# Kernel tuning notes

Hardware: AMD Instinct MI355X
Metric: run time of the kernel (lower is better)

Reference implementation:

```python
import jax, jax.numpy as jnp
import numpy as np

HEADS = 24
HEAD_DIM = 96
SPARSE_N = 4
ROPE_BASE = 10000.0


def _rope_cos_sin(pos, D):
    # pos: [L] int positions; D: per-axis rotary dim (even)
    inv_freq = 1.0 / (ROPE_BASE ** (jnp.arange(0, D, 2, dtype=jnp.float32) / D))
    f = pos.astype(jnp.float32)[:, None] * inv_freq[None, :]   # [L, D/2] (interp scale = 1)
    f = jnp.concatenate([f, f], axis=-1)                        # [L, D]
    return jnp.cos(f), jnp.sin(f)


def _rotate_half(x):
    x1, x2 = jnp.split(x, 2, axis=-1)
    return jnp.concatenate([-x2, x1], axis=-1)


def _apply_rope3d(tok, frame, height, width):
    # tok: [b, h, s, d]; RoPE3D splits head_dim into 3 equal chunks for (t, y, x)
    D = tok.shape[-1] // 3
    t = jnp.repeat(jnp.arange(frame), height * width)
    y = jnp.tile(jnp.repeat(jnp.arange(height), width), frame)
    x = jnp.tile(jnp.arange(width), frame * height)
    outs = []
    for i, pos in enumerate((t, y, x)):
        cos, sin = _rope_cos_sin(pos, D)                        # [s, D]
        part = tok[..., i * D:(i + 1) * D]
        outs.append(part * cos[None, None] + _rotate_half(part) * sin[None, None])
    return jnp.concatenate(outs, axis=-1)


def _sparse_1d(x, n):
    # 'b h (g k) d -> (k b) h g d' with pad so s % n*n == 0
    b, h, s, d = x.shape
    pad = (-s) % (n * n)
    if pad:
        x = jnp.pad(x, ((0, 0), (0, 0), (0, pad), (0, 0)))
    g = (s + pad) // n
    x = x.reshape(b, h, g, n, d)
    return jnp.transpose(x, (3, 0, 1, 2, 4)).reshape(n * b, h, g, d), pad


def _reverse_sparse_1d(x, n, s):
    # '(k b) h g d -> b h (g k) d' then crop to s tokens
    kb, h, g, d = x.shape
    b = kb // n
    x = x.reshape(n, b, h, g, d)
    x = jnp.transpose(x, (1, 2, 3, 0, 4)).reshape(b, h, g * n, d)
    return x[:, :, :s, :]


def setup_inputs() -> dict:
    key = jax.random.key(0)
    ks = jax.random.split(key, 5)
    dim = HEADS * HEAD_DIM
    b, f, hh, ww = 1, 8, 16, 32
    s = f * hh * ww
    inp = {
        "hidden_states": jax.random.normal(ks[0], (b, s, dim), dtype=jnp.float32),
        "wq": jax.random.normal(ks[1], (dim, dim), dtype=jnp.float32) * 0.02,
        "bq": jnp.zeros((dim,), jnp.float32),
        "wk": jax.random.normal(ks[2], (dim, dim), dtype=jnp.float32) * 0.02,
        "bk": jnp.zeros((dim,), jnp.float32),
        "wv": jax.random.normal(ks[3], (dim, dim), dtype=jnp.float32) * 0.02,
        "bv": jnp.zeros((dim,), jnp.float32),
        "wo": jax.random.normal(ks[4], (dim, dim), dtype=jnp.float32) * 0.02,
        "bo": jnp.zeros((dim,), jnp.float32),
        "frame": f, "height": hh, "width": ww,
    }
    return inp


def reference(hidden_states, wq, bq, wk, bk, wv, bv, wo, bo, frame, height, width):
    b, s, dim = hidden_states.shape
    assert s == frame * height * width

    def proj(w, bias):
        y = hidden_states @ w + bias                            # [b, s, dim]
        return jnp.transpose(y.reshape(b, s, HEADS, HEAD_DIM), (0, 2, 1, 3))  # [b, h, s, d]

    q = proj(wq, bq)
    k = proj(wk, bk)
    v = proj(wv, bv)

    # 3D rotary embedding on q, k (self-attention path)
    q = _apply_rope3d(q, frame, height, width)
    k = _apply_rope3d(k, frame, height, width)

    # sparse-1d grouping (sparse_group=False): strided token groups of size s/sparse_n
    q, _ = _sparse_1d(q, SPARSE_N)
    k, _ = _sparse_1d(k, SPARSE_N)
    v, _ = _sparse_1d(v, SPARSE_N)

    scale = 1.0 / jnp.sqrt(jnp.asarray(HEAD_DIM, jnp.float32))
    scores = jnp.einsum('bhqd,bhkd->bhqk', q, k) * scale        # [(n b), h, g, g]
    probs = jax.nn.softmax(scores, axis=-1)
    out = jnp.einsum('bhqk,bhkd->bhqd', probs, v)

    out = _reverse_sparse_1d(out, SPARSE_N, s)                   # [b, h, s, d]
    out = jnp.transpose(out, (0, 2, 1, 3)).reshape(b, s, dim)
    return out @ wo + bo
```

## Files before the change

kernel.cpp:

```cpp
#include <hip/hip_runtime.h>
#include <stdint.h>

#define S_TOK 4096
#define DIM   2304
#define NH    24
#define DH    96
#define GQ    1024
#define KDIM  2304

typedef unsigned short ushort_t;
typedef __attribute__((ext_vector_type(8))) short bf16x8;
typedef __attribute__((ext_vector_type(4))) float f32x4;

__device__ __forceinline__ ushort_t f2bf(float x) {
    union { float f; uint32_t u; } c; c.f = x;
    uint32_t u = c.u + 0x7FFFu + ((c.u >> 16) & 1u);
    return (ushort_t)(u >> 16);
}

#define GLDS(gp, lp) __builtin_amdgcn_global_load_lds( \
    (const __attribute__((address_space(1))) void*)(gp), \
    (__attribute__((address_space(3))) void*)(lp), 16, 0, 0)

__global__ __launch_bounds__(256) void cast_bf16_kernel(const float* __restrict__ in,
                                                        ushort_t* __restrict__ out, int n4) {
    int i = blockIdx.x * 256 + threadIdx.x;
    if (i >= n4) return;
    float4 v = ((const float4*)in)[i];
    ushort4 o;
    o.x = f2bf(v.x); o.y = f2bf(v.y); o.z = f2bf(v.z); o.w = f2bf(v.w);
    ((ushort4*)out)[i] = o;
}

__global__ __launch_bounds__(256) void wtrans_kernel(const float* __restrict__ W0,
                                                     const float* __restrict__ W1,
                                                     const float* __restrict__ W2,
                                                     const float* __restrict__ W3,
                                                     ushort_t* __restrict__ WT0, int dim) {
    __shared__ float tile[32][33];
    const int z = blockIdx.z;
    const float* W = (z == 0) ? W0 : (z == 1) ? W1 : (z == 2) ? W2 : W3;
    ushort_t* WT = WT0 + (size_t)z * dim * dim;
    const int bx = blockIdx.x * 32;
    const int by = blockIdx.y * 32;
    const int tx = threadIdx.x & 31, ty = threadIdx.x >> 5;
#pragma unroll
    for (int i = 0; i < 4; ++i)
        tile[ty + i*8][tx] = W[(size_t)(by + ty + i*8) * dim + bx + tx];
    __syncthreads();
#pragma unroll
    for (int i = 0; i < 4; ++i)
        WT[(size_t)(bx + ty + i*8) * dim + by + tx] = f2bf(tile[tx][ty + i*8]);
}

template<bool FINAL>
__global__ __launch_bounds__(512, 2) void gemm256(const ushort_t* __restrict__ A,
                                                  const ushort_t* __restrict__ Bt,
                                                  const float* __restrict__ bq,
                                                  const float* __restrict__ bk,
                                                  const float* __restrict__ bv,
                                                  ushort_t* __restrict__ Qb,
                                                  ushort_t* __restrict__ Kb,
                                                  ushort_t* __restrict__ Vtb,
                                                  float* __restrict__ Cf) {
    constexpr int K  = KDIM;
    constexpr int NT = K / 32;
    __shared__ ushort_t a_s[4 * 8192];
    __shared__ ushort_t b_s[4 * 8192];
    const int t = threadIdx.x, l = t & 63, w = t >> 6;
    const int wr = w >> 2, wc = w & 3, g = l >> 4, ln = l & 15;
    const int nwg = gridDim.x * gridDim.y;
    const int lin = blockIdx.y * gridDim.x + blockIdx.x;
    const int cpx = nwg >> 3;
    const int swz = (lin & 7) * cpx + (lin >> 3);
    const int bx = swz % gridDim.x, by = swz / gridDim.x;
    const int m0 = by * 256, n0 = bx * 256;

    const int swz_rd = (g ^ ((ln >> 1) & 3)) * 8;
    const int kc_src = (((t & 3) ^ ((t >> 3) & 3)) * 8);
    const int srow   = t >> 2;

    auto stageA = [&](int kt) {
        const int slot = kt & 3;
#pragma unroll
        for (int q = 0; q < 2; ++q)
            GLDS(A + (size_t)(m0 + q*128 + srow) * K + kt*32 + kc_src,
                 &a_s[slot*8192 + (q*512 + t) * 8]);
    };
    auto stageB = [&](int kt) {
        const int slot = kt & 3;
#pragma unroll
        for (int q = 0; q < 2; ++q)
            GLDS(Bt + (size_t)(n0 + q*128 + srow) * K + kt*32 + kc_src,
                 &b_s[slot*8192 + (q*512 + t) * 8]);
    };

    f32x4 acc[8][4] = {};

    stageA(0); stageB(0); stageA(1); stageB(1); stageA(2); stageB(2);
    asm volatile("s_waitcnt vmcnt(8)" ::: "memory");
    __builtin_amdgcn_s_barrier();

    for (int kt = 0; kt < NT; ++kt) {
        const int slot = kt & 3;
        bf16x8 bv4[4];
        {
            bf16x8 av[4];
#pragma unroll
            for (int j = 0; j < 4; ++j)
                bv4[j] = *(const bf16x8*)&b_s[slot*8192 + (wc*64 + j*16 + ln)*32 + swz_rd];
#pragma unroll
            for (int i = 0; i < 4; ++i)
                av[i] = *(const bf16x8*)&a_s[slot*8192 + (wr*128 + i*16 + ln)*32 + swz_rd];
            if (kt < NT - 3) stageA(kt + 3);
            __builtin_amdgcn_s_barrier();
            asm volatile("s_waitcnt lgkmcnt(0)" ::: "memory");
            __builtin_amdgcn_sched_barrier(0);
            __builtin_amdgcn_s_setprio(1);
#pragma unroll
            for (int i = 0; i < 4; ++i)
#pragma unroll
                for (int j = 0; j < 4; ++j)
                    acc[i][j] = __builtin_amdgcn_mfma_f32_16x16x32_bf16(av[i], bv4[j], acc[i][j], 0, 0, 0);
            __builtin_amdgcn_s_setprio(0);
        }
        {
            bf16x8 av[4];
#pragma unroll
            for (int i = 0; i < 4; ++i)
                av[i] = *(const bf16x8*)&a_s[slot*8192 + (wr*128 + 64 + i*16 + ln)*32 + swz_rd];
            if (kt < NT - 3) stageB(kt + 3);
            if (kt <= NT - 4)      asm volatile("s_waitcnt vmcnt(8)" ::: "memory");
            else if (kt == NT - 3) asm volatile("s_waitcnt vmcnt(4)" ::: "memory");
            else                   asm volatile("s_waitcnt vmcnt(0)" ::: "memory");
            __builtin_amdgcn_s_barrier();
            asm volatile("s_waitcnt lgkmcnt(0)" ::: "memory");
            __builtin_amdgcn_sched_barrier(0);
            __builtin_amdgcn_s_setprio(1);
#pragma unroll
            for (int i = 0; i < 4; ++i)
#pragma unroll
                for (int j = 0; j < 4; ++j)
                    acc[4 + i][j] = __builtin_amdgcn_mfma_f32_16x16x32_bf16(av[i], bv4[j], acc[4 + i][j], 0, 0, 0);
            __builtin_amdgcn_s_setprio(0);
        }
    }

    if constexpr (FINAL) {
        const float* bias = bq;
#pragma unroll
        for (int i = 0; i < 8; ++i) {
            int mb = m0 + wr*128 + i*16 + g*4;
#pragma unroll
            for (int j = 0; j < 4; ++j) {
                int n = n0 + wc*64 + j*16 + ln;
                float bb = bias[n];
#pragma unroll
                for (int r = 0; r < 4; ++r)
                    Cf[(size_t)(mb + r) * DIM + n] = acc[i][j][r] + bb;
            }
        }
    } else {
        const int mode = bx / 9;
        const int nb = (bx - mode * 9) * 256;
        const float* bias = (mode == 0) ? bq : (mode == 1) ? bk : bv;
        if (mode == 2) {
#pragma unroll
            for (int i = 0; i < 8; ++i) {
                int mb = m0 + wr*128 + i*16 + g*4;
                int q  = mb >> 2;
#pragma unroll
                for (int j = 0; j < 4; ++j) {
                    int nm = nb + wc*64 + j*16 + ln;
                    int hh = nm / DH, d = nm - hh * DH;
                    float bb = bias[nm];
#pragma unroll
                    for (int r = 0; r < 4; ++r)
                        Vtb[(size_t)(r * NH + hh) * (DH * GQ) + (size_t)d * GQ + q] =
                            f2bf(acc[i][j][r] + bb);
                }
            }
        } else {
            ushort_t* O = (mode == 0) ? Qb : Kb;
            const float scq = (mode == 0) ? 0.1472444635222742f : 1.0f;
#pragma unroll
            for (int i = 0; i < 8; ++i) {
                int mb = m0 + wr*128 + i*16 + g*4;
#pragma unroll
                for (int jp = 0; jp < 2; ++jp) {
                    int j  = jp * 2;
                    int n1 = nb + wc*64 + j*16 + ln;
                    int hh = n1 / DH, d1 = n1 - hh * DH;
                    int sec = d1 >> 5, f = d1 & 15;
                    float invf = __expf((float)f * -0.5756462732485114f);
                    float b1 = bias[n1], b2 = bias[n1 + 16];
#pragma unroll
                    for (int r = 0; r < 4; ++r) {
                        int m = mb + r;
                        int pos = (sec == 0) ? (m >> 9) : (sec == 1) ? ((m >> 5) & 15) : (m & 31);
                        float ang = (float)pos * invf;
                        float sn, cs;
                        __sincosf(ang, &sn, &cs);
                        float v1 = acc[i][j][r]     + b1;
                        float v2 = acc[i][j + 1][r] + b2;
                        size_t base = ((size_t)((m & 3) * NH + hh)) * (GQ * DH) + (size_t)(m >> 2) * DH;
                        O[base + d1]      = f2bf((v1 * cs - v2 * sn) * scq);
                        O[base + d1 + 16] = f2bf((v2 * cs + v1 * sn) * scq);
                    }
                }
            }
        }
    }
}

__global__ __launch_bounds__(256) void gemm128(const ushort_t* __restrict__ A,
                                               const ushort_t* __restrict__ Bt,
                                               const float* __restrict__ bias,
                                               float* __restrict__ C) {
    constexpr int K  = KDIM;
    constexpr int NT = K / 32;
    __shared__ ushort_t a_s[2 * 4096];
    __shared__ ushort_t b_s[2 * 4096];
    const int t = threadIdx.x;
    const int l = t & 63, w = t >> 6;
    const int wr = w >> 1, wc = w & 1;
    const int g = l >> 4, ln = l & 15;
    const int lin = blockIdx.y * gridDim.x + blockIdx.x;
    const int swz = (lin & 7) * 72 + (lin >> 3);
    const int bx = swz % 18, by = swz / 18;
    const int m0 = by * 128, n0 = bx * 128;

    const int swz_rd = (g ^ ((ln >> 1) & 3)) * 8;
    const int kc_src = (((t & 3) ^ ((t >> 3) & 3)) * 8);
    const int srow   = t >> 2;

    const ushort_t* Ab = A  + (size_t)(m0 + srow) * K + kc_src;
    const ushort_t* Bb = Bt + (size_t)(n0 + srow) * K + kc_src;
    const size_t rstep = (size_t)64 * K;

    auto stage = [&](int kt) {
        const int slot = kt & 1;
        GLDS(Ab + kt*32,         &a_s[slot*4096 + t*8]);
        GLDS(Ab + rstep + kt*32, &a_s[slot*4096 + 2048 + t*8]);
        GLDS(Bb + kt*32,         &b_s[slot*4096 + t*8]);
        GLDS(Bb + rstep + kt*32, &b_s[slot*4096 + 2048 + t*8]);
    };

    f32x4 acc[4][4] = {};

    stage(0); stage(1);
    asm volatile("s_waitcnt vmcnt(4)" ::: "memory");
    __builtin_amdgcn_s_barrier();

    for (int kt = 0; kt < NT; ++kt) {
        const int slot = kt & 1;
        bf16x8 av[4], bv[4];
#pragma unroll
        for (int i = 0; i < 4; ++i)
            av[i] = *(const bf16x8*)&a_s[slot*4096 + (wr*64 + i*16 + ln) * 32 + swz_rd];
#pragma unroll
        for (int j = 0; j < 4; ++j)
            bv[j] = *(const bf16x8*)&b_s[slot*4096 + (wc*64 + j*16 + ln) * 32 + swz_rd];
        asm volatile("s_waitcnt lgkmcnt(0)" ::: "memory");
        __builtin_amdgcn_sched_barrier(0);
        __builtin_amdgcn_s_barrier();
        if (kt < NT - 2) {
            stage(kt + 2);
            asm volatile("s_waitcnt vmcnt(4)" ::: "memory");
        } else {
            asm volatile("s_waitcnt vmcnt(0)" ::: "memory");
        }
        __builtin_amdgcn_sched_barrier(0);
        __builtin_amdgcn_s_setprio(1);
#pragma unroll
        for (int i = 0; i < 4; ++i)
#pragma unroll
            for (int j = 0; j < 4; ++j)
                acc[i][j] = __builtin_amdgcn_mfma_f32_16x16x32_bf16(av[i], bv[j], acc[i][j], 0, 0, 0);
        __builtin_amdgcn_s_setprio(0);
        __builtin_amdgcn_sched_barrier(0);
        __builtin_amdgcn_s_barrier();
    }

#pragma unroll
    for (int i = 0; i < 4; ++i) {
        int mb = m0 + wr*64 + i*16 + g*4;
#pragma unroll
        for (int j = 0; j < 4; ++j) {
            int n = n0 + wc*64 + j*16 + ln;
            float bb = bias[n];
#pragma unroll
            for (int r = 0; r < 4; ++r)
                C[(size_t)(mb + r) * DIM + n] = acc[i][j][r] + bb;
        }
    }
}

__global__ __launch_bounds__(256, 3) void attn_kernel(const ushort_t* __restrict__ Qb,
                                                      const ushort_t* __restrict__ Kb,
                                                      const ushort_t* __restrict__ Vt,
                                                      ushort_t* __restrict__ ATT) {
    __shared__ ushort_t k_s[2][12 * 64 * 8];
    __shared__ ushort_t v_s[8 * 96 * 8];
    __shared__ ushort_t p_s[4 * 2 * 16 * 64];

    const int t = threadIdx.x, l = t & 63, w = t >> 6, g = l >> 4, ln = l & 15;
    const int lin  = blockIdx.x;
    const int swz  = (lin & 7) * 96 + (lin >> 3);
    const int inst = swz >> 3;
    const int qb0  = (swz & 7) * 128;
    const int n_idx = inst / NH, h = inst - n_idx * NH;
    const int swzp = (ln & 7) << 3;

    const ushort_t* Qi = Qb + (size_t)inst * (GQ * DH);
    const ushort_t* Ki = Kb + (size_t)inst * (GQ * DH);
    const ushort_t* Vi = Vt + (size_t)inst * (DH * GQ);

    auto stageK = [&](int kt, int b) {
#pragma unroll
        for (int it = 0; it < 3; ++it) {
            int P = t + it * 256;
            int c = P >> 6, key = P & 63;
            GLDS(Ki + (size_t)(kt * 64 + key) * DH + c * 8, &k_s[b][P * 8]);
        }
    };
    auto stageV = [&](int kt) {
#pragma unroll
        for (int it = 0; it < 3; ++it) {
            int P = t + it * 256;
            int c = P / 96, d = P - c * 96;
            GLDS(Vi + (size_t)d * GQ + kt * 64 + c * 8, &v_s[P * 8]);
        }
    };

    bf16x8 qf[2][3];
#pragma unroll
    for (int qt = 0; qt < 2; ++qt)
#pragma unroll
        for (int ks = 0; ks < 3; ++ks)
            qf[qt][ks] = *(const bf16x8*)(Qi + (size_t)(qb0 + w*32 + qt*16 + ln) * DH + ks*32 + g*8);

    float m_run[2], l_run[2];
#pragma unroll
    for (int qt = 0; qt < 2; ++qt) { m_run[qt] = -3.0e38f; l_run[qt] = 0.f; }
    f32x4 acc_o[2][6] = {};

    stageK(0, 0);
    stageV(0);
    __syncthreads();

    int cur = 0;
    for (int kt = 0; kt < 16; ++kt) {
        stageK((kt + 1) & 15, cur ^ 1);
        float al2[2];
        bool grew[2];

        f32x4 sc[2][4] = {};
        __builtin_amdgcn_s_setprio(1);
#pragma unroll
        for (int ct = 0; ct < 4; ++ct) {
            bf16x8 kf0 = *(const bf16x8*)&k_s[cur][((0*4 + g)*64 + ct*16 + ln) * 8];
            bf16x8 kf1 = *(const bf16x8*)&k_s[cur][((1*4 + g)*64 + ct*16 + ln) * 8];
            bf16x8 kf2 = *(const bf16x8*)&k_s[cur][((2*4 + g)*64 + ct*16 + ln) * 8];
#pragma unroll
            for (int qi = 0; qi < 2; ++qi) {
                sc[qi][ct] = __builtin_amdgcn_mfma_f32_16x16x32_bf16(kf0, qf[qi][0], sc[qi][ct], 0, 0, 0);
                sc[qi][ct] = __builtin_amdgcn_mfma_f32_16x16x32_bf16(kf1, qf[qi][1], sc[qi][ct], 0, 0, 0);
                sc[qi][ct] = __builtin_amdgcn_mfma_f32_16x16x32_bf16(kf2, qf[qi][2], sc[qi][ct], 0, 0, 0);
            }
        }
        __builtin_amdgcn_s_setprio(0);
#pragma unroll
        for (int qi = 0; qi < 2; ++qi) {
            const int qt = qi;
            float mx = sc[qi][0][0];
#pragma unroll
            for (int ct = 0; ct < 4; ++ct)
#pragma unroll
                for (int r = 0; r < 4; ++r)
                    mx = fmaxf(mx, sc[qi][ct][r]);
            mx = fmaxf(mx, __shfl_xor(mx, 16, 64));
            mx = fmaxf(mx, __shfl_xor(mx, 32, 64));
            bool grow = !__all(mx <= m_run[qt]);
            float al = 1.0f;
            if (grow) {
                float mn = fmaxf(m_run[qt], mx);
                al = __builtin_amdgcn_exp2f(m_run[qt] - mn);
                m_run[qt] = mn;
            }
            grew[qi] = grow;
            float rs = 0.f;
            ushort_t pb[16];
#pragma unroll
            for (int ct = 0; ct < 4; ++ct)
#pragma unroll
                for (int r = 0; r < 4; ++r) {
                    float p = __builtin_amdgcn_exp2f(sc[qi][ct][r] - m_run[qt]);
                    rs += p;
                    pb[ct*4 + r] = f2bf(p);
                }
            rs += __shfl_xor(rs, 16, 64);
            rs += __shfl_xor(rs, 32, 64);
            l_run[qt] = l_run[qt] * al + rs;
            al2[qt] = al;
            const int pbase = ((w*2 + qt)*16 + ln) * 64;
#pragma unroll
            for (int ct = 0; ct < 4; ++ct) {
                ushort4 pk;
                pk.x = pb[ct*4+0]; pk.y = pb[ct*4+1]; pk.z = pb[ct*4+2]; pk.w = pb[ct*4+3];
                *(ushort4*)&p_s[pbase + ((ct*16 + g*4) ^ swzp)] = pk;
            }
        }

        if (grew[0] || grew[1]) {
#pragma unroll
            for (int qt = 0; qt < 2; ++qt)
#pragma unroll
                for (int r = 0; r < 4; ++r) {
                    float a = __shfl(al2[qt], g*4 + r, 16);
#pragma unroll
                    for (int dt = 0; dt < 6; ++dt)
                        acc_o[qt][dt][r] *= a;
                }
        }

        asm volatile("s_waitcnt vmcnt(3)" ::: "memory");
        __builtin_amdgcn_s_barrier();
        __builtin_amdgcn_sched_barrier(0);
        asm volatile("s_waitcnt lgkmcnt(0)" ::: "memory");
        __builtin_amdgcn_sched_barrier(0);

        __builtin_amdgcn_s_setprio(1);
#pragma unroll
        for (int kb = 0; kb < 2; ++kb) {
            bf16x8 pf2[2];
#pragma unroll
            for (int qt = 0; qt < 2; ++qt)
                pf2[qt] = *(const bf16x8*)&p_s[((w*2 + qt)*16 + ln)*64 + ((kb*32 + g*8) ^ swzp)];
#pragma unroll
            for (int dt = 0; dt < 6; ++dt) {
                bf16x8 vf = *(const bf16x8*)&v_s[((kb*4 + g)*96 + dt*16 + ln) * 8];
#pragma unroll
                for (int qt = 0; qt < 2; ++qt)
                    acc_o[qt][dt] = __builtin_amdgcn_mfma_f32_16x16x32_bf16(pf2[qt], vf, acc_o[qt][dt], 0, 0, 0);
            }
        }
        __builtin_amdgcn_s_setprio(0);

        __syncthreads();
        if (kt < 15) stageV(kt + 1);
        cur ^= 1;
    }

#pragma unroll
    for (int qt = 0; qt < 2; ++qt) {
        float inv = 1.0f / l_run[qt];
#pragma unroll
        for (int r = 0; r < 4; ++r) {
            float iv = __shfl(inv, g*4 + r, 16);
            int gq = qb0 + w*32 + qt*16 + g*4 + r;
            size_t base = ((size_t)(gq * 4 + n_idx)) * DIM + h * DH;
#pragma unroll
            for (int dt = 0; dt < 6; ++dt)
                ATT[base + dt*16 + ln] = f2bf(acc_o[qt][dt][r] * iv);
        }
    }
}

extern "C" void kernel_launch(void* const* d_in, const int* in_sizes, int n_in,
                              void* d_out, int out_size, void* d_ws, size_t ws_size,
                              hipStream_t stream) {
    const float* hidden = (const float*)d_in[0];
    const float* wq = (const float*)d_in[1];
    const float* bq = (const float*)d_in[2];
    const float* wk = (const float*)d_in[3];
    const float* bk = (const float*)d_in[4];
    const float* wv = (const float*)d_in[5];
    const float* bv = (const float*)d_in[6];
    const float* wo = (const float*)d_in[7];
    const float* bo = (const float*)d_in[8];
    float* out = (float*)d_out;

    char* ws = (char*)d_ws;
    ushort_t* Xb  = (ushort_t*)ws;
    ushort_t* WTq = (ushort_t*)(ws + 18874368);
    ushort_t* WTk = WTq + (size_t)DIM * DIM;
    ushort_t* WTv = WTk + (size_t)DIM * DIM;
    ushort_t* WTo = WTv + (size_t)DIM * DIM;
    ushort_t* Qb  = WTo + (size_t)DIM * DIM;
    ushort_t* Kb  = Qb + (size_t)S_TOK * DIM;
    ushort_t* Vtb = Kb + (size_t)S_TOK * DIM;
    ushort_t* ATT = Vtb + (size_t)S_TOK * DIM;

    cast_bf16_kernel<<<dim3(9216), dim3(256), 0, stream>>>(hidden, Xb, (S_TOK * DIM) / 4);

    wtrans_kernel<<<dim3(72, 72, 4), 256, 0, stream>>>(wq, wk, wv, wo, WTq, DIM);

    gemm256<false><<<dim3(27, 16), 512, 0, stream>>>(Xb, WTq, bq, bk, bv, Qb, Kb, Vtb, nullptr);

    attn_kernel<<<dim3(768), 256, 0, stream>>>(Qb, Kb, Vtb, ATT);

    gemm128<<<dim3(18, 32), 256, 0, stream>>>(ATT, WTo, bo, out);
}
```

Before: 325.9 us.

## Replace 256x256 QKV GEMM with 128x128 tiled kernel and double buffering

The fused QKV projection GEMM moves from 256x256 tiles with 512 threads and a 4-stage LDS pipeline to 128x128 tiles with 256 threads, a 2-stage pipeline, and 4 blocks per CU. This raises the block count from 432 to 1728 so the 256 CUs are filled more evenly, with less tail imbalance. In exchange, each tile gets less operand reuse, so global and L2 traffic rises, and the shallower pipeline may hide latency less well. The RoPE, scaling and scatter epilogue is kept the same, with indices adapted to the smaller tile.

```diff
diff --git a/kernel.cpp b/kernel.cpp
--- a/kernel.cpp
+++ b/kernel.cpp
@@ -53,160 +53,124 @@
         WT[(size_t)(bx + ty + i*8) * dim + by + tx] = f2bf(tile[tx][ty + i*8]);
 }
 
-template<bool FINAL>
-__global__ __launch_bounds__(512, 2) void gemm256(const ushort_t* __restrict__ A,
-                                                  const ushort_t* __restrict__ Bt,
-                                                  const float* __restrict__ bq,
-                                                  const float* __restrict__ bk,
-                                                  const float* __restrict__ bv,
-                                                  ushort_t* __restrict__ Qb,
-                                                  ushort_t* __restrict__ Kb,
-                                                  ushort_t* __restrict__ Vtb,
-                                                  float* __restrict__ Cf) {
+__global__ __launch_bounds__(256, 4) void gemm128_qkv(const ushort_t* __restrict__ A,
+                                                      const ushort_t* __restrict__ Bt,
+                                                      const float* __restrict__ bq,
+                                                      const float* __restrict__ bk,
+                                                      const float* __restrict__ bv,
+                                                      ushort_t* __restrict__ Qb,
+                                                      ushort_t* __restrict__ Kb,
+                                                      ushort_t* __restrict__ Vtb) {
     constexpr int K  = KDIM;
     constexpr int NT = K / 32;
-    __shared__ ushort_t a_s[4 * 8192];
-    __shared__ ushort_t b_s[4 * 8192];
-    const int t = threadIdx.x, l = t & 63, w = t >> 6;
-    const int wr = w >> 2, wc = w & 3, g = l >> 4, ln = l & 15;
-    const int nwg = gridDim.x * gridDim.y;
+    __shared__ ushort_t a_s[2 * 4096];
+    __shared__ ushort_t b_s[2 * 4096];
+    const int t = threadIdx.x;
+    const int l = t & 63, w = t >> 6;
+    const int wr = w >> 1, wc = w & 1;
+    const int g = l >> 4, ln = l & 15;
     const int lin = blockIdx.y * gridDim.x + blockIdx.x;
-    const int cpx = nwg >> 3;
-    const int swz = (lin & 7) * cpx + (lin >> 3);
-    const int bx = swz % gridDim.x, by = swz / gridDim.x;
-    const int m0 = by * 256, n0 = bx * 256;
+    const int swz = (lin & 7) * 216 + (lin >> 3);
+    const int bx = swz % 54, by = swz / 54;
+    const int m0 = by * 128, n0g = bx * 128;
 
     const int swz_rd = (g ^ ((ln >> 1) & 3)) * 8;
     const int kc_src = (((t & 3) ^ ((t >> 3) & 3)) * 8);
     const int srow   = t >> 2;
 
-    auto stageA = [&](int kt) {
-        const int slot = kt & 3;
-#pragma unroll
-        for (int q = 0; q < 2; ++q)
-            GLDS(A + (size_t)(m0 + q*128 + srow) * K + kt*32 + kc_src,
-                 &a_s[slot*8192 + (q*512 + t) * 8]);
+    const ushort_t* Ab = A  + (size_t)(m0  + srow) * K + kc_src;
+    const ushort_t* Bb = Bt + (size_t)(n0g + srow) * K + kc_src;
+    const size_t rstep = (size_t)64 * K;
+
+    auto stage = [&](int kt) {
+        const int slot = kt & 1;
+        GLDS(Ab + kt*32,         &a_s[slot*4096 + t*8]);
+        GLDS(Ab + rstep + kt*32, &a_s[slot*4096 + 2048 + t*8]);
+        GLDS(Bb + kt*32,         &b_s[slot*4096 + t*8]);
+        GLDS(Bb + rstep + kt*32, &b_s[slot*4096 + 2048 + t*8]);
     };
-    auto stageB = [&](int kt) {
-        const int slot = kt & 3;
-#pragma unroll
-        for (int q = 0; q < 2; ++q)
-            GLDS(Bt + (size_t)(n0 + q*128 + srow) * K + kt*32 + kc_src,
-                 &b_s[slot*8192 + (q*512 + t) * 8]);
-    };
-
-    f32x4 acc[8][4] = {};
-
-    stageA(0); stageB(0); stageA(1); stageB(1); stageA(2); stageB(2);
-    asm volatile("s_waitcnt vmcnt(8)" ::: "memory");
+
+    f32x4 acc[4][4] = {};
+
+    stage(0); stage(1);
+    asm volatile("s_waitcnt vmcnt(4)" ::: "memory");
     __builtin_amdgcn_s_barrier();
 
     for (int kt = 0; kt < NT; ++kt) {
-        const int slot = kt & 3;
-        bf16x8 bv4[4];
-        {
-            bf16x8 av[4];
+        const int slot = kt & 1;
+        bf16x8 av[4], bv4[4];
+#pragma unroll
+        for (int i = 0; i < 4; ++i)
+            av[i] = *(const bf16x8*)&a_s[slot*4096 + (wr*64 + i*16 + ln) * 32 + swz_rd];
+#pragma unroll
+        for (int j = 0; j < 4; ++j)
+            bv4[j] = *(const bf16x8*)&b_s[slot*4096 + (wc*64 + j*16 + ln) * 32 + swz_rd];
+        asm volatile("s_waitcnt lgkmcnt(0)" ::: "memory");
+        __builtin_amdgcn_sched_barrier(0);
+        __builtin_amdgcn_s_barrier();
+        if (kt < NT - 2) {
+            stage(kt + 2);
+            asm volatile("s_waitcnt vmcnt(4)" ::: "memory");
+        } else {
+            asm volatile("s_waitcnt vmcnt(0)" ::: "memory");
+        }
+        __builtin_amdgcn_sched_barrier(0);
+        __builtin_amdgcn_s_setprio(1);
+#pragma unroll
+        for (int i = 0; i < 4; ++i)
 #pragma unroll
             for (int j = 0; j < 4; ++j)
-                bv4[j] = *(const bf16x8*)&b_s[slot*8192 + (wc*64 + j*16 + ln)*32 + swz_rd];
-#pragma unroll
-            for (int i = 0; i < 4; ++i)
-                av[i] = *(const bf16x8*)&a_s[slot*8192 + (wr*128 + i*16 + ln)*32 + swz_rd];
-            if (kt < NT - 3) stageA(kt + 3);
-            __builtin_amdgcn_s_barrier();
-            asm volatile("s_waitcnt lgkmcnt(0)" ::: "memory");
-            __builtin_amdgcn_sched_barrier(0);
-            __builtin_amdgcn_s_setprio(1);
-#pragma unroll
-            for (int i = 0; i < 4; ++i)
-#pragma unroll
-                for (int j = 0; j < 4; ++j)
-                    acc[i][j] = __builtin_amdgcn_mfma_f32_16x16x32_bf16(av[i], bv4[j], acc[i][j], 0, 0, 0);
-            __builtin_amdgcn_s_setprio(0);
-        }
-        {
-            bf16x8 av[4];
-#pragma unroll
-            for (int i = 0; i < 4; ++i)
-                av[i] = *(const bf16x8*)&a_s[slot*8192 + (wr*128 + 64 + i*16 + ln)*32 + swz_rd];
-            if (kt < NT - 3) stageB(kt + 3);
-            if (kt <= NT - 4)      asm volatile("s_waitcnt vmcnt(8)" ::: "memory");
-            else if (kt == NT - 3) asm volatile("s_waitcnt vmcnt(4)" ::: "memory");
-            else                   asm volatile("s_waitcnt vmcnt(0)" ::: "memory");
-            __builtin_amdgcn_s_barrier();
-            asm volatile("s_waitcnt lgkmcnt(0)" ::: "memory");
-            __builtin_amdgcn_sched_barrier(0);
-            __builtin_amdgcn_s_setprio(1);
-#pragma unroll
-            for (int i = 0; i < 4; ++i)
-#pragma unroll
-                for (int j = 0; j < 4; ++j)
-                    acc[4 + i][j] = __builtin_amdgcn_mfma_f32_16x16x32_bf16(av[i], bv4[j], acc[4 + i][j], 0, 0, 0);
-            __builtin_amdgcn_s_setprio(0);
-        }
-    }
-
-    if constexpr (FINAL) {
-        const float* bias = bq;
-#pragma unroll
-        for (int i = 0; i < 8; ++i) {
-            int mb = m0 + wr*128 + i*16 + g*4;
+                acc[i][j] = __builtin_amdgcn_mfma_f32_16x16x32_bf16(av[i], bv4[j], acc[i][j], 0, 0, 0);
+        __builtin_amdgcn_s_setprio(0);
+        __builtin_amdgcn_sched_barrier(0);
+        __builtin_amdgcn_s_barrier();
+    }
+
+    const int mode = bx / 18;
+    const int nb = (bx - mode * 18) * 128;
+    const float* bias = (mode == 0) ? bq : (mode == 1) ? bk : bv;
+    if (mode == 2) {
+#pragma unroll
+        for (int i = 0; i < 4; ++i) {
+            int mb = m0 + wr*64 + i*16 + g*4;
+            int q  = mb >> 2;
 #pragma unroll
             for (int j = 0; j < 4; ++j) {
-                int n = n0 + wc*64 + j*16 + ln;
-                float bb = bias[n];
+                int nm = nb + wc*64 + j*16 + ln;
+                int hh = nm / DH, d = nm - hh * DH;
+                float bb = bias[nm];
 #pragma unroll
                 for (int r = 0; r < 4; ++r)
-                    Cf[(size_t)(mb + r) * DIM + n] = acc[i][j][r] + bb;
+                    Vtb[(size_t)(r * NH + hh) * (DH * GQ) + (size_t)d * GQ + q] =
+                        f2bf(acc[i][j][r] + bb);
             }
         }
     } else {
-        const int mode = bx / 9;
-        const int nb = (bx - mode * 9) * 256;
-        const float* bias = (mode == 0) ? bq : (mode == 1) ? bk : bv;
-        if (mode == 2) {
-#pragma unroll
-            for (int i = 0; i < 8; ++i) {
-                int mb = m0 + wr*128 + i*16 + g*4;
-                int q  = mb >> 2;
-#pragma unroll
-                for (int j = 0; j < 4; ++j) {
-                    int nm = nb + wc*64 + j*16 + ln;
-                    int hh = nm / DH, d = nm - hh * DH;
-                    float bb = bias[nm];
-#pragma unroll
-                    for (int r = 0; r < 4; ++r)
-                        Vtb[(size_t)(r * NH + hh) * (DH * GQ) + (size_t)d * GQ + q] =
-                            f2bf(acc[i][j][r] + bb);
-                }
-            }
-        } else {
-            ushort_t* O = (mode == 0) ? Qb : Kb;
-            const float scq = (mode == 0) ? 0.1472444635222742f : 1.0f;
-#pragma unroll
-            for (int i = 0; i < 8; ++i) {
-                int mb = m0 + wr*128 + i*16 + g*4;
-#pragma unroll
-                for (int jp = 0; jp < 2; ++jp) {
-                    int j  = jp * 2;
-                    int n1 = nb + wc*64 + j*16 + ln;
-                    int hh = n1 / DH, d1 = n1 - hh * DH;
-                    int sec = d1 >> 5, f = d1 & 15;
-                    float invf = __expf((float)f * -0.5756462732485114f);
-                    float b1 = bias[n1], b2 = bias[n1 + 16];
-#pragma unroll
-                    for (int r = 0; r < 4; ++r) {
-                        int m = mb + r;
-                        int pos = (sec == 0) ? (m >> 9) : (sec == 1) ? ((m >> 5) & 15) : (m & 31);
-                        float ang = (float)pos * invf;
-                        float sn, cs;
-                        __sincosf(ang, &sn, &cs);
-                        float v1 = acc[i][j][r]     + b1;
-                        float v2 = acc[i][j + 1][r] + b2;
-                        size_t base = ((size_t)((m & 3) * NH + hh)) * (GQ * DH) + (size_t)(m >> 2) * DH;
-                        O[base + d1]      = f2bf((v1 * cs - v2 * sn) * scq);
-                        O[base + d1 + 16] = f2bf((v2 * cs + v1 * sn) * scq);
-                    }
+        ushort_t* O = (mode == 0) ? Qb : Kb;
+        const float scq = (mode == 0) ? 0.1472444635222742f : 1.0f;
+#pragma unroll
+        for (int i = 0; i < 4; ++i) {
+            int mb = m0 + wr*64 + i*16 + g*4;
+#pragma unroll
+            for (int jp = 0; jp < 2; ++jp) {
+                int j  = jp * 2;
+                int n1 = nb + wc*64 + j*16 + ln;
+                int hh = n1 / DH, d1 = n1 - hh * DH;
+                int sec = d1 >> 5, f = d1 & 15;
+                float invf = __expf((float)f * -0.5756462732485114f);
+                float b1 = bias[n1], b2 = bias[n1 + 16];
+#pragma unroll
+                for (int r = 0; r < 4; ++r) {
+                    int m = mb + r;
+                    int pos = (sec == 0) ? (m >> 9) : (sec == 1) ? ((m >> 5) & 15) : (m & 31);
+                    float ang = (float)pos * invf;
+                    float sn, cs;
+                    __sincosf(ang, &sn, &cs);
+                    float v1 = acc[i][j][r]     + b1;
+                    float v2 = acc[i][j + 1][r] + b2;
+                    size_t base = ((size_t)((m & 3) * NH + hh)) * (GQ * DH) + (size_t)(m >> 2) * DH;
+                    O[base + d1]      = f2bf((v1 * cs - v2 * sn) * scq);
+                    O[base + d1 + 16] = f2bf((v2 * cs + v1 * sn) * scq);
                 }
             }
         }
@@ -496,7 +460,7 @@
 
     wtrans_kernel<<<dim3(72, 72, 4), 256, 0, stream>>>(wq, wk, wv, wo, WTq, DIM);
 
-    gemm256<false><<<dim3(27, 16), 512, 0, stream>>>(Xb, WTq, bq, bk, bv, Qb, Kb, Vtb, nullptr);
+    gemm128_qkv<<<dim3(54, 32), 256, 0, stream>>>(Xb, WTq, bq, bk, bv, Qb, Kb, Vtb);
 
     attn_kernel<<<dim3(768), 256, 0, stream>>>(Qb, Kb, Vtb, ATT);
 
```

Result: slower. 345.1 us (+5.9%).
